# Kernel tuning notes

Measured on AMD Instinct MI355X. Metric: run time of the kernel, lower is better.

Reference implementation:

```python
import jax, jax.numpy as jnp
import numpy as np

THRESHOLD = 0.1  # init kwarg threshold
N_HITS_PER_EVENT = 200000
N_EVENTS = 64


def setup_inputs() -> dict:
    key = jax.random.key(0)
    n = N_HITS_PER_EVENT * N_EVENTS
    score = jax.random.uniform(key, (n, 1), dtype=jnp.float32)  # noise score in (0,1)
    row_splits = (jnp.arange(N_EVENTS + 1, dtype=jnp.int32) * N_HITS_PER_EVENT)
    return {"score": score, "row_splits": row_splits}


def reference(score, row_splits):
    """Faithful, fully vectorized version of select_threshold_with_backgather.

    Per segment: keep all vertices with score > threshold PLUS all vertices tied
    with the segment minimum score; non-kept vertices backgather to the FIRST
    kept minimum-score vertex of their segment (new/compacted indexing).
    Returns (sel [M,1], newrs [n_seg+1], backgather [N,1]) in the layer's
    call-output order (sel, newrs, allbackgather).
    """
    s = score[:, 0]
    n = s.shape[0]
    n_seg = row_splits.shape[0] - 1

    # segment id of every vertex from the row splits
    segids = jnp.searchsorted(row_splits, jnp.arange(n, dtype=row_splits.dtype), side='right') - 1
    segids = segids.astype(jnp.int32)

    # per-segment minimum score; ties with the min are all kept (== original isminscore)
    segmin = jax.ops.segment_min(s, segids, num_segments=n_seg)
    ismin = s == segmin[segids]
    keep = (s > THRESHOLD) | ismin

    # global compacted position of each kept vertex (n_previous_rs + local keeprange)
    kept_pos = jnp.cumsum(keep.astype(jnp.int32)) - 1

    # representative = first kept min-score vertex per segment (original minidx + n_previous_rs)
    big = jnp.int32(n)
    rep_pos = jax.ops.segment_min(jnp.where(keep & ismin, kept_pos, big), segids, num_segments=n_seg)

    backgather = jnp.where(keep, kept_pos, rep_pos[segids])

    # selection indices (data-dependent size; computed on concrete values, not under jit)
    sel = jnp.nonzero(keep)[0].astype(jnp.int32)

    counts = jax.ops.segment_sum(keep.astype(jnp.int32), segids, num_segments=n_seg)
    newrs = jnp.concatenate([jnp.zeros((1,), jnp.int32), jnp.cumsum(counts).astype(jnp.int32)])

    return sel[:, None], newrs, backgather[:, None].astype(jnp.int32)
```

## Files before the change

### kernel.cpp

```cpp
#include <hip/hip_runtime.h>
#include <stdint.h>

#define BLOCK 256
#define ITEMS 8
#define TILE (BLOCK * ITEMS)
#define WPB (TILE / 64)
#define MAXSEG 64
#define CHUNK 64
#define NCMAX 128
#define SEGSTRIDE 16
#define CHSTRIDE 32
#define THRESH 0.1f

typedef unsigned long long u64;

__device__ __forceinline__ int find_seg(const int* rs, int n_seg, int i) {
    int lo = 0, hi = n_seg;
    while (hi - lo > 1) {
        int mid = (lo + hi) >> 1;
        if (rs[mid] <= i) lo = mid; else hi = mid;
    }
    return lo;
}

__device__ __forceinline__ int wave_prefix_at(int idx, const int* chq,
        const int* __restrict__ bc, const u64* __restrict__ bm, int lane) {
    int t = idx / TILE;
    int c = t / CHUNK;
    int v = 0;
    int j = c * CHUNK + lane;
    if (j < t) v += bc[j];
    int wq = idx >> 6;
    int w = t * WPB + lane;
    if (lane < WPB && w < wq) v += __popcll(bm[w]);
    if (lane == 0 && (idx & 63)) v += __popcll(bm[wq] & ((1ull << (idx & 63)) - 1));
    for (int o = 32; o > 0; o >>= 1) v += __shfl_down(v, o, 64);
    return chq[c] + v;
}

__global__ __launch_bounds__(BLOCK) void k_pass1(const float* __restrict__ score,
        const int* __restrict__ row_splits, int n_seg, int n, int nwords,
        u64* __restrict__ partial_val, int* __restrict__ partial_seg,
        u64* __restrict__ bitmask, int* __restrict__ block_counts,
        u64* __restrict__ seg_packed, int* __restrict__ chunk_sums) {
    __shared__ int rs[MAXSEG + 1];
    __shared__ u64 wval[8];
    __shared__ int wseg[8];
    __shared__ int wsum[4];
    for (int j = threadIdx.x; j <= n_seg; j += BLOCK) rs[j] = row_splits[j];
    __syncthreads();
    int lane = threadIdx.x & 63, wv = threadIdx.x >> 6;
    int wbase = blockIdx.x * TILE + wv * 512;
    u64 m0 = ~0ull, m1 = ~0ull;
    int sf = -1, sl = -1, cnt = 0;
    if (wbase < n) {
        int wend = min(n, wbase + 512) - 1;
        sf = find_seg(rs, n_seg, wbase);
        sl = find_seg(rs, n_seg, wend);
        int bval = (sl != sf) ? rs[sf + 1] : 0x7FFFFFFF;
        int tbase = wbase + lane * 8;
        unsigned int kbyte = 0;
        if (tbase < n) {
            float v[8];
            if (tbase + 8 <= n) {
                float4 f0 = *(const float4*)(score + tbase);
                float4 f1 = *(const float4*)(score + tbase + 4);
                v[0]=f0.x; v[1]=f0.y; v[2]=f0.z; v[3]=f0.w;
                v[4]=f1.x; v[5]=f1.y; v[6]=f1.z; v[7]=f1.w;
            } else {
                for (int j = 0; j < 8; j++) v[j] = (tbase + j < n) ? score[tbase + j] : 1.0f;
            }
            #pragma unroll
            for (int j = 0; j < 8; j++) {
                int i = tbase + j;
                if (i < n) {
                    u64 p = ((u64)__float_as_uint(v[j]) << 32) | (unsigned int)i;
                    if (i < bval) m0 = min(m0, p); else m1 = min(m1, p);
                    if (v[j] > THRESH) kbyte |= 1u << j;
                }
            }
            cnt = __popc(kbyte);
        }
        u64 acc = ((u64)kbyte) << (8 * (lane & 7));
        acc |= __shfl_xor((unsigned long long)acc, 1, 64);
        acc |= __shfl_xor((unsigned long long)acc, 2, 64);
        acc |= __shfl_xor((unsigned long long)acc, 4, 64);
        int src = (lane < 8) ? (8 * lane) : lane;
        u64 myword = __shfl((unsigned long long)acc, src, 64);
        for (int o = 32; o > 0; o >>= 1) {
            m0 = min(m0, (u64)__shfl_down((unsigned long long)m0, o, 64));
            m1 = min(m1, (u64)__shfl_down((unsigned long long)m1, o, 64));
            cnt += __shfl_down(cnt, o, 64);
        }
        if (lane < 8) {
            int w = (wbase >> 6) + lane;
            if (w < nwords) bitmask[w] = myword;
        }
    }
    if (lane == 0) {
        wval[2 * wv] = m0;     wseg[2 * wv] = sf;
        wval[2 * wv + 1] = m1; wseg[2 * wv + 1] = (sl != sf) ? sl : -1;
        wsum[wv] = (wbase < n) ? cnt : 0;
    }
    __syncthreads();
    if (threadIdx.x == 0) {
        int base = blockIdx.x * TILE;
        int endi = min(n, base + TILE) - 1;
        int s0 = find_seg(rs, n_seg, base);
        int s1 = find_seg(rs, n_seg, endi);
        u64 o0 = ~0ull, o1 = ~0ull;
        for (int k = 0; k < 8; k++) {
            if (wseg[k] == s0) o0 = min(o0, wval[k]);
            else if (wseg[k] == s1) o1 = min(o1, wval[k]);
        }
        partial_val[2 * blockIdx.x] = o0;
        partial_seg[2 * blockIdx.x] = s0;
        partial_val[2 * blockIdx.x + 1] = o1;
        partial_seg[2 * blockIdx.x + 1] = (s1 != s0) ? s1 : -1;
        int bc = wsum[0] + wsum[1] + wsum[2] + wsum[3];
        block_counts[blockIdx.x] = bc;
        atomicMin(&seg_packed[SEGSTRIDE * s0], o0);
        if (s1 != s0) atomicMin(&seg_packed[SEGSTRIDE * s1], o1);
        atomicAdd(&chunk_sums[CHSTRIDE * (blockIdx.x / CHUNK)], bc);
    }
}

__global__ __launch_bounds__(BLOCK) void k_segfix(const float* __restrict__ score,
        const int* __restrict__ row_splits, int n,
        const u64* __restrict__ partial_val, const int* __restrict__ partial_seg,
        const u64* __restrict__ seg_packed, u64* __restrict__ bitmask,
        int* __restrict__ block_counts, int* __restrict__ chunk_sums) {
    __shared__ int nmatch;
    __shared__ int mlist[64];
    int s = blockIdx.x;
    int lo = row_splits[s], hi = row_splits[s + 1];
    int lane = threadIdx.x & 63;
    if (threadIdx.x == 0) nmatch = 0;
    __syncthreads();
    if (hi <= lo) return;
    u64 sp = seg_packed[SEGSTRIDE * s];
    if (sp == ~0ull) return;
    unsigned int smb = (unsigned int)(sp >> 32);
    if (__uint_as_float(smb) > THRESH) return;
    int e0 = 2 * (lo / TILE);
    int e1 = 2 * ((hi - 1) / TILE) + 1;
    for (int e = e0 + threadIdx.x; e <= e1; e += BLOCK) {
        if (partial_seg[e] == s && (unsigned int)(partial_val[e] >> 32) == smb) {
            int k = atomicAdd(&nmatch, 1);
            if (k < 64) mlist[k] = e >> 1;
        }
    }
    __syncthreads();
    int nm = min(nmatch, 64);
    for (int k = 0; k < nm; k++) {
        int b = mlist[k];
        int rlo = max(b * TILE, lo);
        int rhi = min(min((b + 1) * TILE, n), hi);
        int c = 0;
        for (int i = rlo + threadIdx.x; i < rhi; i += BLOCK) {
            if (__float_as_uint(score[i]) == smb) {
                atomicOr(&bitmask[i >> 6], 1ull << (i & 63));
                c++;
            }
        }
        for (int o = 32; o > 0; o >>= 1) c += __shfl_down(c, o, 64);
        if (lane == 0 && c) {
            atomicAdd(&block_counts[b], c);
            atomicAdd(&chunk_sums[CHSTRIDE * (b / CHUNK)], c);
        }
    }
}

__global__ __launch_bounds__(BLOCK) void k_output(const int* __restrict__ row_splits,
        int n_seg, int n, int nb, int nchunk, int M,
        const u64* __restrict__ seg_packed, const u64* __restrict__ bitmask,
        const int* __restrict__ block_counts, const int* __restrict__ chunk_sums,
        int* __restrict__ sel_out, int* __restrict__ back_out,
        int* __restrict__ newrs_out) {
    __shared__ int rs[MAXSEG + 1];
    __shared__ u64 swords[WPB];
    __shared__ int wpre[WPB];
    __shared__ int shead[8];
    __shared__ int chq[NCMAX];
    __shared__ alignas(16) int skel[TILE + 8];
    for (int j = threadIdx.x; j <= n_seg; j += BLOCK) rs[j] = row_splits[j];
    int base = blockIdx.x * TILE;
    int lim = min(TILE, n - base);
    int nw = (lim + 63) >> 6;
    for (int j = threadIdx.x; j < nw; j += BLOCK) swords[j] = bitmask[(base >> 6) + j];
    __syncthreads();
    int lane = threadIdx.x & 63, wv = threadIdx.x >> 6;
    if (wv == 0) {
        int c0 = 2 * lane, c1 = 2 * lane + 1;
        int a = (c0 < nchunk) ? chunk_sums[CHSTRIDE * c0] + 1 : 0;
        int b2 = (c1 < nchunk) ? chunk_sums[CHSTRIDE * c1] + 1 : 0;
        int ps = a + b2;
        int incl = ps;
        for (int o = 1; o < 64; o <<= 1) {
            int t = __shfl_up(incl, o, 64);
            if (lane >= o) incl += t;
        }
        int excl = incl - ps;
        if (c0 < nchunk) chq[c0] = excl;
        if (c1 < nchunk) chq[c1] = excl + a;
    } else if (threadIdx.x == 64) {
        int acc = 0;
        for (int k = 0; k < nw; k++) { wpre[k] = acc; acc += __popcll(swords[k]); }
        int s0 = find_seg(rs, n_seg, base);
        int s1 = find_seg(rs, n_seg, base + lim - 1);
        shead[0] = (s1 != s0) ? rs[s0 + 1] : 0x7FFFFFFF;
        shead[1] = s0;
        shead[2] = s1;
        shead[3] = acc;
    }
    __syncthreads();
    {
        int s0 = shead[1], s1 = shead[2];
        if (wv == 0) {
            int r = wave_prefix_at(base, chq, block_counts, bitmask, lane);
            if (lane == 0) shead[4] = r;
        } else if (wv == 1) {
            unsigned int u = (unsigned int)(seg_packed[SEGSTRIDE * s0] & 0xFFFFFFFFu);
            int r = (u >= (unsigned int)n) ? M
                    : wave_prefix_at((int)u, chq, block_counts, bitmask, lane);
            if (lane == 0) shead[5] = r;
        } else if (wv == 2) {
            unsigned int u = (unsigned int)(seg_packed[SEGSTRIDE * s1] & 0xFFFFFFFFu);
            int r = (u >= (unsigned int)n) ? M
                    : wave_prefix_at((int)u, chq, block_counts, bitmask, lane);
            if (lane == 0) shead[6] = r;
        } else {
            for (int q = 0; q < n_seg; q++) {
                int u = rs[q];
                if (u >= base && u < base + lim) {
                    int r = wave_prefix_at(u, chq, block_counts, bitmask, lane);
                    if (lane == 0) newrs_out[q] = r;
                }
            }
            if (blockIdx.x == nb - 1 && lane == 0) newrs_out[n_seg] = M;
        }
    }
    __syncthreads();
    int bval = shead[0], tot = shead[3], bo = shead[4];
    int rep0 = shead[5], rep1 = shead[6];
    int st_b = (int)((4 - ((((uintptr_t)(back_out + base)) >> 2) & 3)) & 3);
    if (st_b > lim) st_b = lim;
    int st_s = (int)((4 - ((((uintptr_t)(sel_out + bo)) >> 2) & 3)) & 3);
    if (st_s > tot) st_s = tot;
    int selpad = 4 - st_s;

    int ngroups = (lim - st_b) >> 2;
    for (int g = threadIdx.x; g < ngroups; g += BLOCK) {
        int j0 = st_b + 4 * g;
        int vals[4];
        #pragma unroll
        for (int k = 0; k < 4; k++) {
            int j = j0 + k;
            int widx = j >> 6, r = j & 63;
            u64 w = swords[widx];
            int i = base + j;
            if ((w >> r) & 1) {
                int pos = bo + wpre[widx] + __popcll(w & ((1ull << r) - 1));
                vals[k] = pos;
                skel[pos - bo + selpad] = i;
            } else {
                vals[k] = (i >= bval) ? rep1 : rep0;
            }
        }
        *(int4*)(back_out + base + j0) = make_int4(vals[0], vals[1], vals[2], vals[3]);
    }
    for (int j = threadIdx.x; j < st_b; j += BLOCK) {
        int widx = j >> 6, r = j & 63;
        u64 w = swords[widx];
        int i = base + j, val;
        if ((w >> r) & 1) {
            int pos = bo + wpre[widx] + __popcll(w & ((1ull << r) - 1));
            val = pos;
            skel[pos - bo + selpad] = i;
        } else val = (i >= bval) ? rep1 : rep0;
        back_out[i] = val;
    }
    for (int j = st_b + 4 * ngroups + threadIdx.x; j < lim; j += BLOCK) {
        int widx = j >> 6, r = j & 63;
        u64 w = swords[widx];
        int i = base + j, val;
        if ((w >> r) & 1) {
            int pos = bo + wpre[widx] + __popcll(w & ((1ull << r) - 1));
            val = pos;
            skel[pos - bo + selpad] = i;
        } else val = (i >= bval) ? rep1 : rep0;
        back_out[i] = val;
    }
    __syncthreads();
    int nvg = (tot - st_s) >> 2;
    for (int g = threadIdx.x; g < nvg; g += BLOCK) {
        int4 v = *(const int4*)&skel[4 + 4 * g];
        *(int4*)(sel_out + bo + st_s + 4 * g) = v;
    }
    for (int j = threadIdx.x; j < st_s; j += BLOCK) sel_out[bo + j] = skel[j + selpad];
    for (int j = st_s + 4 * nvg + threadIdx.x; j < tot; j += BLOCK) sel_out[bo + j] = skel[j + selpad];
}

extern "C" void kernel_launch(void* const* d_in, const int* in_sizes, int n_in,
                              void* d_out, int out_size, void* d_ws, size_t ws_size,
                              hipStream_t stream) {
    const float* score = (const float*)d_in[0];
    const int* row_splits = (const int*)d_in[1];
    int n = in_sizes[0];
    int n_seg = in_sizes[1] - 1;
    int M = out_size - (n_seg + 1) - n;
    int nb = (n + TILE - 1) / TILE;
    int nwords = (n + 63) / 64;
    int nchunk = (nb + CHUNK - 1) / CHUNK;

    u64* seg_packed   = (u64*)d_ws;
    int* chunk_sums   = (int*)(seg_packed + MAXSEG * SEGSTRIDE);
    uintptr_t pv_addr = (uintptr_t)(chunk_sums + (size_t)nchunk * CHSTRIDE);
    pv_addr = (pv_addr + 7) & ~(uintptr_t)7;
    u64* partial_val  = (u64*)pv_addr;
    int* partial_seg  = (int*)(partial_val + 2 * nb);
    int* block_counts = partial_seg + 2 * nb;
    uintptr_t bm_addr = (uintptr_t)(block_counts + nb);
    bm_addr = (bm_addr + 7) & ~(uintptr_t)7;
    u64* bitmask      = (u64*)bm_addr;

    int* out = (int*)d_out;
    int* sel_out   = out;
    int* newrs_out = out + M;
    int* back_out  = out + M + (n_seg + 1);

    size_t init_bytes = (size_t)((char*)(chunk_sums + (size_t)nchunk * CHSTRIDE) - (char*)d_ws);
    hipMemsetAsync(d_ws, 0xFF, init_bytes, stream);
    hipLaunchKernelGGL(k_pass1, dim3(nb), dim3(BLOCK), 0, stream,
                       score, row_splits, n_seg, n, nwords,
                       partial_val, partial_seg, bitmask, block_counts,
                       seg_packed, chunk_sums);
    hipLaunchKernelGGL(k_segfix, dim3(n_seg), dim3(BLOCK), 0, stream,
                       score, row_splits, n,
                       partial_val, partial_seg, seg_packed, bitmask,
                       block_counts, chunk_sums);
    hipLaunchKernelGGL(k_output, dim3(nb), dim3(BLOCK), 0, stream,
                       row_splits, n_seg, n, nb, nchunk, M,
                       seg_packed, bitmask, block_counts, chunk_sums,
                       sel_out, back_out, newrs_out);
}
```

Baseline: 180.5 us.

## Fuse three kernels into one persistent kernel with grid barriers

Replaces the pass1, segfix and output kernels with a single persistent kernel launched at an occupancy-sized grid. Its blocks loop over tiles and synchronise through a global atomic counter barrier, with memset-initialised counters. Loads that cross the barriers go through atomic read-modify-write operations to stay coherent. The aim is to remove two kernel launch gaps and the tail effects between them. In exchange it adds barrier spinning, slower atomic loads and stores for the bitmask, partials and counts, and a risk of deadlock if not every block is co-resident.

```diff
diff --git a/kernel.cpp b/kernel.cpp
--- a/kernel.cpp
+++ b/kernel.cpp
@@ -14,6 +14,9 @@
 
 typedef unsigned long long u64;
 
+__device__ __forceinline__ u64 aload64(u64* p) { return atomicAdd(p, 0ull); }
+__device__ __forceinline__ int aload32(int* p) { return atomicAdd(p, 0); }
+
 __device__ __forceinline__ int find_seg(const int* rs, int n_seg, int i) {
     int lo = 0, hi = n_seg;
     while (hi - lo > 1) {
@@ -23,282 +26,293 @@
     return lo;
 }
 
-__device__ __forceinline__ int wave_prefix_at(int idx, const int* chq,
-        const int* __restrict__ bc, const u64* __restrict__ bm, int lane) {
-    int t = idx / TILE;
-    int c = t / CHUNK;
+__device__ __forceinline__ void grid_bar(int* ctr, int target) {
+    __syncthreads();
+    if (threadIdx.x == 0) {
+        __asm__ volatile("s_waitcnt vmcnt(0)" ::: "memory");
+        atomicAdd(ctr, 1);
+        while (aload32(ctr) < target) __builtin_amdgcn_s_sleep(8);
+    }
+    __syncthreads();
+}
+
+__device__ __forceinline__ int wpa(int idx, const int* chq, int* bc,
+                                   u64* bm, int lane) {
+    int t = idx / TILE, c = t / CHUNK;
     int v = 0;
     int j = c * CHUNK + lane;
-    if (j < t) v += bc[j];
+    if (j < t) v += aload32(&bc[j]);
     int wq = idx >> 6;
     int w = t * WPB + lane;
-    if (lane < WPB && w < wq) v += __popcll(bm[w]);
-    if (lane == 0 && (idx & 63)) v += __popcll(bm[wq] & ((1ull << (idx & 63)) - 1));
+    if (lane < WPB && w < wq) v += __popcll(aload64(&bm[w]));
+    if (lane == 0 && (idx & 63)) v += __popcll(aload64(&bm[wq]) & ((1ull << (idx & 63)) - 1));
     for (int o = 32; o > 0; o >>= 1) v += __shfl_down(v, o, 64);
     return chq[c] + v;
 }
 
-__global__ __launch_bounds__(BLOCK) void k_pass1(const float* __restrict__ score,
-        const int* __restrict__ row_splits, int n_seg, int n, int nwords,
-        u64* __restrict__ partial_val, int* __restrict__ partial_seg,
-        u64* __restrict__ bitmask, int* __restrict__ block_counts,
-        u64* __restrict__ seg_packed, int* __restrict__ chunk_sums) {
+__global__ __launch_bounds__(BLOCK) void k_fused(const float* __restrict__ score,
+        const int* __restrict__ row_splits, int n_seg, int n, int nb,
+        int nwords, int nchunk, int M, int G,
+        u64* partial_val, int* partial_seg, u64* bitmask, int* block_counts,
+        u64* seg_packed, int* chunk_sums, int* ctr,
+        int* __restrict__ sel_out, int* __restrict__ back_out,
+        int* __restrict__ newrs_out) {
     __shared__ int rs[MAXSEG + 1];
     __shared__ u64 wval[8];
     __shared__ int wseg[8];
     __shared__ int wsum[4];
+    __shared__ int nmatch;
+    __shared__ int mlist[64];
+    __shared__ u64 swords[WPB];
+    __shared__ int wpre[WPB];
+    __shared__ int shead[8];
+    __shared__ int qidx[4];
+    __shared__ int chq[NCMAX];
+    __shared__ alignas(16) int skel[TILE + 8];
+
     for (int j = threadIdx.x; j <= n_seg; j += BLOCK) rs[j] = row_splits[j];
     __syncthreads();
     int lane = threadIdx.x & 63, wv = threadIdx.x >> 6;
-    int wbase = blockIdx.x * TILE + wv * 512;
-    u64 m0 = ~0ull, m1 = ~0ull;
-    int sf = -1, sl = -1, cnt = 0;
-    if (wbase < n) {
-        int wend = min(n, wbase + 512) - 1;
-        sf = find_seg(rs, n_seg, wbase);
-        sl = find_seg(rs, n_seg, wend);
-        int bval = (sl != sf) ? rs[sf + 1] : 0x7FFFFFFF;
-        int tbase = wbase + lane * 8;
-        unsigned int kbyte = 0;
-        if (tbase < n) {
-            float v[8];
-            if (tbase + 8 <= n) {
-                float4 f0 = *(const float4*)(score + tbase);
-                float4 f1 = *(const float4*)(score + tbase + 4);
-                v[0]=f0.x; v[1]=f0.y; v[2]=f0.z; v[3]=f0.w;
-                v[4]=f1.x; v[5]=f1.y; v[6]=f1.z; v[7]=f1.w;
-            } else {
-                for (int j = 0; j < 8; j++) v[j] = (tbase + j < n) ? score[tbase + j] : 1.0f;
-            }
-            #pragma unroll
-            for (int j = 0; j < 8; j++) {
-                int i = tbase + j;
-                if (i < n) {
-                    u64 p = ((u64)__float_as_uint(v[j]) << 32) | (unsigned int)i;
-                    if (i < bval) m0 = min(m0, p); else m1 = min(m1, p);
-                    if (v[j] > THRESH) kbyte |= 1u << j;
-                }
-            }
-            cnt = __popc(kbyte);
-        }
-        u64 acc = ((u64)kbyte) << (8 * (lane & 7));
-        acc |= __shfl_xor((unsigned long long)acc, 1, 64);
-        acc |= __shfl_xor((unsigned long long)acc, 2, 64);
-        acc |= __shfl_xor((unsigned long long)acc, 4, 64);
-        int src = (lane < 8) ? (8 * lane) : lane;
-        u64 myword = __shfl((unsigned long long)acc, src, 64);
-        for (int o = 32; o > 0; o >>= 1) {
-            m0 = min(m0, (u64)__shfl_down((unsigned long long)m0, o, 64));
-            m1 = min(m1, (u64)__shfl_down((unsigned long long)m1, o, 64));
-            cnt += __shfl_down(cnt, o, 64);
-        }
-        if (lane < 8) {
-            int w = (wbase >> 6) + lane;
-            if (w < nwords) bitmask[w] = myword;
-        }
-    }
-    if (lane == 0) {
-        wval[2 * wv] = m0;     wseg[2 * wv] = sf;
-        wval[2 * wv + 1] = m1; wseg[2 * wv + 1] = (sl != sf) ? sl : -1;
-        wsum[wv] = (wbase < n) ? cnt : 0;
-    }
-    __syncthreads();
-    if (threadIdx.x == 0) {
-        int base = blockIdx.x * TILE;
-        int endi = min(n, base + TILE) - 1;
-        int s0 = find_seg(rs, n_seg, base);
-        int s1 = find_seg(rs, n_seg, endi);
-        u64 o0 = ~0ull, o1 = ~0ull;
-        for (int k = 0; k < 8; k++) {
-            if (wseg[k] == s0) o0 = min(o0, wval[k]);
-            else if (wseg[k] == s1) o1 = min(o1, wval[k]);
-        }
-        partial_val[2 * blockIdx.x] = o0;
-        partial_seg[2 * blockIdx.x] = s0;
-        partial_val[2 * blockIdx.x + 1] = o1;
-        partial_seg[2 * blockIdx.x + 1] = (s1 != s0) ? s1 : -1;
-        int bc = wsum[0] + wsum[1] + wsum[2] + wsum[3];
-        block_counts[blockIdx.x] = bc;
-        atomicMin(&seg_packed[SEGSTRIDE * s0], o0);
-        if (s1 != s0) atomicMin(&seg_packed[SEGSTRIDE * s1], o1);
-        atomicAdd(&chunk_sums[CHSTRIDE * (blockIdx.x / CHUNK)], bc);
-    }
-}
-
-__global__ __launch_bounds__(BLOCK) void k_segfix(const float* __restrict__ score,
-        const int* __restrict__ row_splits, int n,
-        const u64* __restrict__ partial_val, const int* __restrict__ partial_seg,
-        const u64* __restrict__ seg_packed, u64* __restrict__ bitmask,
-        int* __restrict__ block_counts, int* __restrict__ chunk_sums) {
-    __shared__ int nmatch;
-    __shared__ int mlist[64];
-    int s = blockIdx.x;
-    int lo = row_splits[s], hi = row_splits[s + 1];
-    int lane = threadIdx.x & 63;
-    if (threadIdx.x == 0) nmatch = 0;
-    __syncthreads();
-    if (hi <= lo) return;
-    u64 sp = seg_packed[SEGSTRIDE * s];
-    if (sp == ~0ull) return;
-    unsigned int smb = (unsigned int)(sp >> 32);
-    if (__uint_as_float(smb) > THRESH) return;
-    int e0 = 2 * (lo / TILE);
-    int e1 = 2 * ((hi - 1) / TILE) + 1;
-    for (int e = e0 + threadIdx.x; e <= e1; e += BLOCK) {
-        if (partial_seg[e] == s && (unsigned int)(partial_val[e] >> 32) == smb) {
-            int k = atomicAdd(&nmatch, 1);
-            if (k < 64) mlist[k] = e >> 1;
-        }
-    }
-    __syncthreads();
-    int nm = min(nmatch, 64);
-    for (int k = 0; k < nm; k++) {
-        int b = mlist[k];
-        int rlo = max(b * TILE, lo);
-        int rhi = min(min((b + 1) * TILE, n), hi);
-        int c = 0;
-        for (int i = rlo + threadIdx.x; i < rhi; i += BLOCK) {
-            if (__float_as_uint(score[i]) == smb) {
-                atomicOr(&bitmask[i >> 6], 1ull << (i & 63));
-                c++;
-            }
-        }
-        for (int o = 32; o > 0; o >>= 1) c += __shfl_down(c, o, 64);
-        if (lane == 0 && c) {
-            atomicAdd(&block_counts[b], c);
-            atomicAdd(&chunk_sums[CHSTRIDE * (b / CHUNK)], c);
-        }
-    }
-}
-
-__global__ __launch_bounds__(BLOCK) void k_output(const int* __restrict__ row_splits,
-        int n_seg, int n, int nb, int nchunk, int M,
-        const u64* __restrict__ seg_packed, const u64* __restrict__ bitmask,
-        const int* __restrict__ block_counts, const int* __restrict__ chunk_sums,
-        int* __restrict__ sel_out, int* __restrict__ back_out,
-        int* __restrict__ newrs_out) {
-    __shared__ int rs[MAXSEG + 1];
-    __shared__ u64 swords[WPB];
-    __shared__ int wpre[WPB];
-    __shared__ int shead[8];
-    __shared__ int chq[NCMAX];
-    __shared__ alignas(16) int skel[TILE + 8];
-    for (int j = threadIdx.x; j <= n_seg; j += BLOCK) rs[j] = row_splits[j];
-    int base = blockIdx.x * TILE;
-    int lim = min(TILE, n - base);
-    int nw = (lim + 63) >> 6;
-    for (int j = threadIdx.x; j < nw; j += BLOCK) swords[j] = bitmask[(base >> 6) + j];
-    __syncthreads();
-    int lane = threadIdx.x & 63, wv = threadIdx.x >> 6;
+
+    for (int t = blockIdx.x; t < nb; t += G) {
+        int wbase = t * TILE + wv * 512;
+        u64 m0 = ~0ull, m1 = ~0ull;
+        int sf = -1, sl = -1, cnt = 0;
+        if (wbase < n) {
+            int wend = min(n, wbase + 512) - 1;
+            sf = find_seg(rs, n_seg, wbase);
+            sl = find_seg(rs, n_seg, wend);
+            int bval = (sl != sf) ? rs[sf + 1] : 0x7FFFFFFF;
+            int tbase = wbase + lane * 8;
+            unsigned int kbyte = 0;
+            if (tbase < n) {
+                float v[8];
+                if (tbase + 8 <= n) {
+                    float4 f0 = *(const float4*)(score + tbase);
+                    float4 f1 = *(const float4*)(score + tbase + 4);
+                    v[0]=f0.x; v[1]=f0.y; v[2]=f0.z; v[3]=f0.w;
+                    v[4]=f1.x; v[5]=f1.y; v[6]=f1.z; v[7]=f1.w;
+                } else {
+                    for (int j = 0; j < 8; j++) v[j] = (tbase + j < n) ? score[tbase + j] : 1.0f;
+                }
+                #pragma unroll
+                for (int j = 0; j < 8; j++) {
+                    int i = tbase + j;
+                    if (i < n) {
+                        u64 p = ((u64)__float_as_uint(v[j]) << 32) | (unsigned int)i;
+                        if (i < bval) m0 = min(m0, p); else m1 = min(m1, p);
+                        if (v[j] > THRESH) kbyte |= 1u << j;
+                    }
+                }
+                cnt = __popc(kbyte);
+            }
+            u64 acc = ((u64)kbyte) << (8 * (lane & 7));
+            acc |= __shfl_xor((unsigned long long)acc, 1, 64);
+            acc |= __shfl_xor((unsigned long long)acc, 2, 64);
+            acc |= __shfl_xor((unsigned long long)acc, 4, 64);
+            int src = (lane < 8) ? (8 * lane) : lane;
+            u64 myword = __shfl((unsigned long long)acc, src, 64);
+            for (int o = 32; o > 0; o >>= 1) {
+                m0 = min(m0, (u64)__shfl_down((unsigned long long)m0, o, 64));
+                m1 = min(m1, (u64)__shfl_down((unsigned long long)m1, o, 64));
+                cnt += __shfl_down(cnt, o, 64);
+            }
+            if (lane < 8) {
+                int w = (wbase >> 6) + lane;
+                if (w < nwords) atomicExch(&bitmask[w], myword);
+            }
+        }
+        if (lane == 0) {
+            wval[2 * wv] = m0;     wseg[2 * wv] = sf;
+            wval[2 * wv + 1] = m1; wseg[2 * wv + 1] = (sl != sf) ? sl : -1;
+            wsum[wv] = (wbase < n) ? cnt : 0;
+        }
+        __syncthreads();
+        if (threadIdx.x == 0) {
+            int base = t * TILE;
+            int endi = min(n, base + TILE) - 1;
+            int s0 = find_seg(rs, n_seg, base);
+            int s1 = find_seg(rs, n_seg, endi);
+            u64 o0 = ~0ull, o1 = ~0ull;
+            for (int k = 0; k < 8; k++) {
+                if (wseg[k] == s0) o0 = min(o0, wval[k]);
+                else if (wseg[k] == s1) o1 = min(o1, wval[k]);
+            }
+            atomicExch(&partial_val[2 * t], o0);
+            atomicExch(&partial_seg[2 * t], s0);
+            atomicExch(&partial_val[2 * t + 1], o1);
+            atomicExch(&partial_seg[2 * t + 1], (s1 != s0) ? s1 : -1);
+            int bc = wsum[0] + wsum[1] + wsum[2] + wsum[3];
+            atomicExch(&block_counts[t], bc);
+            atomicAdd(&chunk_sums[CHSTRIDE * (t / CHUNK)], bc);
+            atomicMin(&seg_packed[SEGSTRIDE * s0], o0);
+            if (s1 != s0) atomicMin(&seg_packed[SEGSTRIDE * s1], o1);
+        }
+        __syncthreads();
+    }
+    grid_bar(ctr, G - 1);
+
+    if ((int)blockIdx.x < n_seg) {
+        int s = blockIdx.x;
+        int lo = rs[s], hi = rs[s + 1];
+        if (threadIdx.x == 0) nmatch = 0;
+        __syncthreads();
+        if (hi > lo) {
+            u64 sp = aload64(&seg_packed[SEGSTRIDE * s]);
+            unsigned int smb = (unsigned int)(sp >> 32);
+            if (sp != ~0ull && __uint_as_float(smb) <= THRESH) {
+                int e0 = 2 * (lo / TILE), e1 = 2 * ((hi - 1) / TILE) + 1;
+                for (int e = e0 + threadIdx.x; e <= e1; e += BLOCK) {
+                    if (aload32(&partial_seg[e]) == s &&
+                        (unsigned int)(aload64(&partial_val[e]) >> 32) == smb) {
+                        int k = atomicAdd(&nmatch, 1);
+                        if (k < 64) mlist[k] = e >> 1;
+                    }
+                }
+                __syncthreads();
+                int nm = min(nmatch, 64);
+                for (int k = 0; k < nm; k++) {
+                    int b = mlist[k];
+                    int rlo = max(b * TILE, lo);
+                    int rhi = min(min((b + 1) * TILE, n), hi);
+                    int c = 0;
+                    for (int i = rlo + threadIdx.x; i < rhi; i += BLOCK) {
+                        if (__float_as_uint(score[i]) == smb) {
+                            atomicOr(&bitmask[i >> 6], 1ull << (i & 63));
+                            c++;
+                        }
+                    }
+                    for (int o = 32; o > 0; o >>= 1) c += __shfl_down(c, o, 64);
+                    if (lane == 0 && c) {
+                        atomicAdd(&block_counts[b], c);
+                        atomicAdd(&chunk_sums[CHSTRIDE * (b / CHUNK)], c);
+                    }
+                }
+            }
+        }
+    }
+    grid_bar(ctr, 2 * G - 1);
+
     if (wv == 0) {
         int c0 = 2 * lane, c1 = 2 * lane + 1;
-        int a = (c0 < nchunk) ? chunk_sums[CHSTRIDE * c0] + 1 : 0;
-        int b2 = (c1 < nchunk) ? chunk_sums[CHSTRIDE * c1] + 1 : 0;
-        int ps = a + b2;
-        int incl = ps;
+        int a  = (c0 < nchunk) ? aload32(&chunk_sums[CHSTRIDE * c0]) + 1 : 0;
+        int b2 = (c1 < nchunk) ? aload32(&chunk_sums[CHSTRIDE * c1]) + 1 : 0;
+        int ps = a + b2, incl = ps;
         for (int o = 1; o < 64; o <<= 1) {
-            int t = __shfl_up(incl, o, 64);
-            if (lane >= o) incl += t;
+            int tv = __shfl_up(incl, o, 64);
+            if (lane >= o) incl += tv;
         }
         int excl = incl - ps;
         if (c0 < nchunk) chq[c0] = excl;
         if (c1 < nchunk) chq[c1] = excl + a;
-    } else if (threadIdx.x == 64) {
-        int acc = 0;
-        for (int k = 0; k < nw; k++) { wpre[k] = acc; acc += __popcll(swords[k]); }
-        int s0 = find_seg(rs, n_seg, base);
-        int s1 = find_seg(rs, n_seg, base + lim - 1);
-        shead[0] = (s1 != s0) ? rs[s0 + 1] : 0x7FFFFFFF;
-        shead[1] = s0;
-        shead[2] = s1;
-        shead[3] = acc;
     }
     __syncthreads();
-    {
-        int s0 = shead[1], s1 = shead[2];
+
+    for (int t = blockIdx.x; t < nb; t += G) {
+        int base = t * TILE;
+        int lim = min(TILE, n - base);
+        int nw = (lim + 63) >> 6;
+        for (int j = threadIdx.x; j < nw; j += BLOCK)
+            swords[j] = aload64(&bitmask[(base >> 6) + j]);
+        __syncthreads();
+        if (threadIdx.x == 0) {
+            int s0 = find_seg(rs, n_seg, base);
+            int s1 = find_seg(rs, n_seg, base + lim - 1);
+            shead[0] = (s1 != s0) ? rs[s0 + 1] : 0x7FFFFFFF;
+            shead[1] = s0;
+            shead[2] = s1;
+            unsigned int u0 = (unsigned int)(aload64(&seg_packed[SEGSTRIDE * s0]) & 0xFFFFFFFFu);
+            unsigned int u1 = (unsigned int)(aload64(&seg_packed[SEGSTRIDE * s1]) & 0xFFFFFFFFu);
+            qidx[1] = (u0 < (unsigned int)n) ? (int)u0 : -1;
+            qidx[2] = (s1 != s0) ? ((u1 < (unsigned int)n) ? (int)u1 : -1) : qidx[1];
+        } else if (threadIdx.x == 64) {
+            int acc = 0;
+            for (int k = 0; k < nw; k++) { wpre[k] = acc; acc += __popcll(swords[k]); }
+            shead[3] = acc;
+        }
+        __syncthreads();
         if (wv == 0) {
-            int r = wave_prefix_at(base, chq, block_counts, bitmask, lane);
+            int r = wpa(base, chq, block_counts, bitmask, lane);
             if (lane == 0) shead[4] = r;
-        } else if (wv == 1) {
-            unsigned int u = (unsigned int)(seg_packed[SEGSTRIDE * s0] & 0xFFFFFFFFu);
-            int r = (u >= (unsigned int)n) ? M
-                    : wave_prefix_at((int)u, chq, block_counts, bitmask, lane);
-            if (lane == 0) shead[5] = r;
-        } else if (wv == 2) {
-            unsigned int u = (unsigned int)(seg_packed[SEGSTRIDE * s1] & 0xFFFFFFFFu);
-            int r = (u >= (unsigned int)n) ? M
-                    : wave_prefix_at((int)u, chq, block_counts, bitmask, lane);
-            if (lane == 0) shead[6] = r;
-        } else {
-            for (int q = 0; q < n_seg; q++) {
-                int u = rs[q];
-                if (u >= base && u < base + lim) {
-                    int r = wave_prefix_at(u, chq, block_counts, bitmask, lane);
-                    if (lane == 0) newrs_out[q] = r;
-                }
-            }
-            if (blockIdx.x == nb - 1 && lane == 0) newrs_out[n_seg] = M;
-        }
-    }
-    __syncthreads();
-    int bval = shead[0], tot = shead[3], bo = shead[4];
-    int rep0 = shead[5], rep1 = shead[6];
-    int st_b = (int)((4 - ((((uintptr_t)(back_out + base)) >> 2) & 3)) & 3);
-    if (st_b > lim) st_b = lim;
-    int st_s = (int)((4 - ((((uintptr_t)(sel_out + bo)) >> 2) & 3)) & 3);
-    if (st_s > tot) st_s = tot;
-    int selpad = 4 - st_s;
-
-    int ngroups = (lim - st_b) >> 2;
-    for (int g = threadIdx.x; g < ngroups; g += BLOCK) {
-        int j0 = st_b + 4 * g;
-        int vals[4];
-        #pragma unroll
-        for (int k = 0; k < 4; k++) {
-            int j = j0 + k;
+        } else if (wv == 1 || wv == 2) {
+            int qi = qidx[wv];
+            int r;
+            if (qi < 0) r = M;
+            else r = wpa(qi, chq, block_counts, bitmask, lane);
+            if (lane == 0) shead[4 + wv] = r;
+        }
+        __syncthreads();
+        int bval = shead[0], tot = shead[3], bo = shead[4];
+        int rep0 = shead[5], rep1 = shead[6];
+        if (threadIdx.x < n_seg) {
+            int u = rs[threadIdx.x];
+            if (u >= base && u < base + lim) {
+                int j = u - base, widx = j >> 6;
+                int r = bo + wpre[widx] +
+                        ((j & 63) ? __popcll(swords[widx] & ((1ull << (j & 63)) - 1)) : 0);
+                newrs_out[threadIdx.x] = r;
+            }
+        }
+        if (t == nb - 1 && threadIdx.x == 0) newrs_out[n_seg] = M;
+
+        int st_b = (int)((4 - ((((uintptr_t)(back_out + base)) >> 2) & 3)) & 3);
+        if (st_b > lim) st_b = lim;
+        int st_s = (int)((4 - ((((uintptr_t)(sel_out + bo)) >> 2) & 3)) & 3);
+        if (st_s > tot) st_s = tot;
+        int selpad = 4 - st_s;
+
+        int ngroups = (lim - st_b) >> 2;
+        for (int g = threadIdx.x; g < ngroups; g += BLOCK) {
+            int j0 = st_b + 4 * g;
+            int vals[4];
+            #pragma unroll
+            for (int k = 0; k < 4; k++) {
+                int j = j0 + k;
+                int widx = j >> 6, r = j & 63;
+                u64 w = swords[widx];
+                int i = base + j;
+                if ((w >> r) & 1) {
+                    int pos = bo + wpre[widx] + __popcll(w & ((1ull << r) - 1));
+                    vals[k] = pos;
+                    skel[pos - bo + selpad] = i;
+                } else {
+                    vals[k] = (i >= bval) ? rep1 : rep0;
+                }
+            }
+            *(int4*)(back_out + base + j0) = make_int4(vals[0], vals[1], vals[2], vals[3]);
+        }
+        for (int j = threadIdx.x; j < st_b; j += BLOCK) {
             int widx = j >> 6, r = j & 63;
             u64 w = swords[widx];
-            int i = base + j;
+            int i = base + j, val;
             if ((w >> r) & 1) {
                 int pos = bo + wpre[widx] + __popcll(w & ((1ull << r) - 1));
-                vals[k] = pos;
+                val = pos;
                 skel[pos - bo + selpad] = i;
-            } else {
-                vals[k] = (i >= bval) ? rep1 : rep0;
-            }
-        }
-        *(int4*)(back_out + base + j0) = make_int4(vals[0], vals[1], vals[2], vals[3]);
-    }
-    for (int j = threadIdx.x; j < st_b; j += BLOCK) {
-        int widx = j >> 6, r = j & 63;
-        u64 w = swords[widx];
-        int i = base + j, val;
-        if ((w >> r) & 1) {
-            int pos = bo + wpre[widx] + __popcll(w & ((1ull << r) - 1));
-            val = pos;
-            skel[pos - bo + selpad] = i;
-        } else val = (i >= bval) ? rep1 : rep0;
-        back_out[i] = val;
-    }
-    for (int j = st_b + 4 * ngroups + threadIdx.x; j < lim; j += BLOCK) {
-        int widx = j >> 6, r = j & 63;
-        u64 w = swords[widx];
-        int i = base + j, val;
-        if ((w >> r) & 1) {
-            int pos = bo + wpre[widx] + __popcll(w & ((1ull << r) - 1));
-            val = pos;
-            skel[pos - bo + selpad] = i;
-        } else val = (i >= bval) ? rep1 : rep0;
-        back_out[i] = val;
-    }
-    __syncthreads();
-    int nvg = (tot - st_s) >> 2;
-    for (int g = threadIdx.x; g < nvg; g += BLOCK) {
-        int4 v = *(const int4*)&skel[4 + 4 * g];
-        *(int4*)(sel_out + bo + st_s + 4 * g) = v;
-    }
-    for (int j = threadIdx.x; j < st_s; j += BLOCK) sel_out[bo + j] = skel[j + selpad];
-    for (int j = st_s + 4 * nvg + threadIdx.x; j < tot; j += BLOCK) sel_out[bo + j] = skel[j + selpad];
+            } else val = (i >= bval) ? rep1 : rep0;
+            back_out[i] = val;
+        }
+        for (int j = st_b + 4 * ngroups + threadIdx.x; j < lim; j += BLOCK) {
+            int widx = j >> 6, r = j & 63;
+            u64 w = swords[widx];
+            int i = base + j, val;
+            if ((w >> r) & 1) {
+                int pos = bo + wpre[widx] + __popcll(w & ((1ull << r) - 1));
+                val = pos;
+                skel[pos - bo + selpad] = i;
+            } else val = (i >= bval) ? rep1 : rep0;
+            back_out[i] = val;
+        }
+        __syncthreads();
+        int nvg = (tot - st_s) >> 2;
+        for (int g = threadIdx.x; g < nvg; g += BLOCK) {
+            int4 v = *(const int4*)&skel[4 + 4 * g];
+            *(int4*)(sel_out + bo + st_s + 4 * g) = v;
+        }
+        for (int j = threadIdx.x; j < st_s; j += BLOCK) sel_out[bo + j] = skel[j + selpad];
+        for (int j = st_s + 4 * nvg + threadIdx.x; j < tot; j += BLOCK) sel_out[bo + j] = skel[j + selpad];
+        __syncthreads();
+    }
 }
 
 extern "C" void kernel_launch(void* const* d_in, const int* in_sizes, int n_in,
@@ -315,7 +329,8 @@
 
     u64* seg_packed   = (u64*)d_ws;
     int* chunk_sums   = (int*)(seg_packed + MAXSEG * SEGSTRIDE);
-    uintptr_t pv_addr = (uintptr_t)(chunk_sums + (size_t)nchunk * CHSTRIDE);
+    int* ctr          = chunk_sums + NCMAX * CHSTRIDE;
+    uintptr_t pv_addr = (uintptr_t)(ctr + 32);
     pv_addr = (pv_addr + 7) & ~(uintptr_t)7;
     u64* partial_val  = (u64*)pv_addr;
     int* partial_seg  = (int*)(partial_val + 2 * nb);
@@ -329,18 +344,21 @@
     int* newrs_out = out + M;
     int* back_out  = out + M + (n_seg + 1);
 
-    size_t init_bytes = (size_t)((char*)(chunk_sums + (size_t)nchunk * CHSTRIDE) - (char*)d_ws);
+    static int gsize = 0;
+    if (gsize == 0) {
+        int mb = 0;
+        if (hipOccupancyMaxActiveBlocksPerMultiprocessor(&mb, k_fused, BLOCK, 0) != hipSuccess
+            || mb < 1) mb = 1;
+        if (mb > 8) mb = 8;
+        gsize = 256 * mb;
+    }
+    int G = gsize;
+
+    size_t init_bytes = (size_t)((char*)(ctr + 32) - (char*)d_ws);
     hipMemsetAsync(d_ws, 0xFF, init_bytes, stream);
-    hipLaunchKernelGGL(k_pass1, dim3(nb), dim3(BLOCK), 0, stream,
-                       score, row_splits, n_seg, n, nwords,
+    hipLaunchKernelGGL(k_fused, dim3(G), dim3(BLOCK), 0, stream,
+                       score, row_splits, n_seg, n, nb, nwords, nchunk, M, G,
                        partial_val, partial_seg, bitmask, block_counts,
-                       seg_packed, chunk_sums);
-    hipLaunchKernelGGL(k_segfix, dim3(n_seg), dim3(BLOCK), 0, stream,
-                       score, row_splits, n,
-                       partial_val, partial_seg, seg_packed, bitmask,
-                       block_counts, chunk_sums);
-    hipLaunchKernelGGL(k_output, dim3(nb), dim3(BLOCK), 0, stream,
-                       row_splits, n_seg, n, nb, nchunk, M,
-                       seg_packed, bitmask, block_counts, chunk_sums,
+                       seg_packed, chunk_sums, ctr,
                        sel_out, back_out, newrs_out);
 }
```

New measurement: 233.9 us. 1.3x slower.
